# Optimization experiments

Measured on AMD Instinct MI355X. Metric: run time of the kernel, lower is better.

The kernel has to match this reference:

```python
import jax, jax.numpy as jnp
import numpy as np

B, H, S, D = 4, 16, 2048, 64
ROPE_BASE = 10000.0


def _rope(x):
    # Rotate-half RoPE over the last dim, positions along the second-to-last dim.
    d = x.shape[-1]
    s = x.shape[-2]
    inv_freq = 1.0 / (ROPE_BASE ** (jnp.arange(0, d, 2, dtype=jnp.float32) / d))  # [D/2]
    ang = jnp.arange(s, dtype=jnp.float32)[:, None] * inv_freq                    # [S, D/2]
    cos, sin = jnp.cos(ang), jnp.sin(ang)
    x1, x2 = x[..., : d // 2], x[..., d // 2:]
    return jnp.concatenate([x1 * cos - x2 * sin, x1 * sin + x2 * cos], axis=-1).astype(x.dtype)


def setup_inputs() -> dict:
    key = jax.random.key(0)
    kq, kk, kv = jax.random.split(key, 3)
    q = jax.random.normal(kq, (B, H, S, D), dtype=jnp.float32)
    k = jax.random.normal(kk, (B, H, S, D), dtype=jnp.float32)
    v = jax.random.normal(kv, (B, H, S, D), dtype=jnp.float32)
    mask = jnp.tril(jnp.ones((S, S), dtype=bool))  # causal, broadcasts over [B,H,S,S]
    return {"q": q, "k": k, "v": v, "mask": mask}


def reference(q, k, v, mask):
    d_k = q.shape[-1]
    qr = _rope(q)
    kr = _rope(k)
    scores = jnp.einsum('bhqd,bhkd->bhqk', qr, kr) / jnp.sqrt(jnp.asarray(d_k, jnp.float32))
    scores = jnp.where(mask, scores, -jnp.inf)  # masked_fill(mask == False, -inf)
    probs = jax.nn.softmax(scores, axis=-1)
    return jnp.einsum('bhqk,bhkd->bhqd', probs, v)
```

## Files before the change

kernel.cpp:

```cpp
#include <hip/hip_runtime.h>
#include <hip/hip_bf16.h>
#include <math.h>

#define SS 2048
#define DD 64
#define BH 64
#define KT 64
#define NT 256
#define NKT (SS / KT)
#define QTT 128
#define NTA 512
#define NQT (SS / QTT)
#define LQ 72
#define LOG2E 1.4426950408889634f
#define IFS (13.287712379549449f / 32.0f)

typedef __attribute__((ext_vector_type(8))) short s8v;
typedef __attribute__((ext_vector_type(4))) short s4v;
typedef __attribute__((ext_vector_type(4))) float f4v;

__device__ __forceinline__ short f2b(float x) {
  __hip_bfloat16 h = __float2bfloat16(x);
  return *reinterpret_cast<short*>(&h);
}

__device__ __forceinline__ void gload16(const void* g, void* l) {
  __builtin_amdgcn_global_load_lds(
      (const __attribute__((address_space(1))) void*)g,
      (__attribute__((address_space(3))) void*)l, 16, 0, 0);
}

template <int CTRL>
__device__ __forceinline__ float dppf(float x) {
  int i = __builtin_bit_cast(int, x);
  i = __builtin_amdgcn_update_dpp(i, i, CTRL, 0xf, 0xf, false);
  return __builtin_bit_cast(float, i);
}
__device__ __forceinline__ float rowmax16(float x) {
  x = fmaxf(x, dppf<0xB1>(x));
  x = fmaxf(x, dppf<0x4E>(x));
  x = fmaxf(x, dppf<0x124>(x));
  x = fmaxf(x, dppf<0x128>(x));
  return x;
}
__device__ __forceinline__ float rowsum16(float x) {
  x += dppf<0xB1>(x);
  x += dppf<0x4E>(x);
  x += dppf<0x124>(x);
  x += dppf<0x128>(x);
  return x;
}

__device__ __forceinline__ void rope_cs(int pos, int j, float& c, float& s) {
  float inv = exp2f(-(float)j * IFS);
  float ang = (float)pos * inv;
  __sincosf(ang, &s, &c);
}

__global__ __launch_bounds__(NT) void prep_kv_kernel(
    const float* __restrict__ kg, const float* __restrict__ vg,
    short* __restrict__ kr, short* __restrict__ vt) {
  __shared__ float Vs[KT][DD + 1];
  const int b = blockIdx.x;
  const int kt = b & 31;
  const int t = threadIdx.x;
  const size_t ofs = (size_t)b * (KT * DD);
  const float* ktile = kg + ofs;
  short* krt = kr + ofs;

#pragma unroll
  for (int i = 0; i < 8; ++i) {
    int idx = t + i * NT;
    int r = idx >> 5, j = idx & 31;
    float s, c;
    rope_cs(kt * KT + r, j, c, s);
    float x1 = ktile[r * DD + j], x2 = ktile[r * DD + j + 32];
    krt[r * DD + j] = f2b(x1 * c - x2 * s);
    krt[r * DD + j + 32] = f2b(x1 * s + x2 * c);
  }

  const float* vtile = vg + ofs;
#pragma unroll
  for (int i = 0; i < 4; ++i) {
    int s4 = t + i * NT;
    int r = s4 >> 4, c4 = (s4 & 15) * 4;
    float4 v = *(const float4*)&vtile[r * DD + c4];
    Vs[r][c4 + 0] = v.x;
    Vs[r][c4 + 1] = v.y;
    Vs[r][c4 + 2] = v.z;
    Vs[r][c4 + 3] = v.w;
  }
  __syncthreads();
  short* otile = vt + ofs;
#pragma unroll
  for (int i = 0; i < 2; ++i) {
    int c = t + i * NT;
    int d = c >> 3, k8 = (c & 7) * 8;
    s8v o;
#pragma unroll
    for (int u = 0; u < 8; ++u) {
      int kp = k8 + u;
      int src = ((kp & 3) << 4) + (kp >> 2);
      o[u] = f2b(Vs[src][d]);
    }
    *(s8v*)&otile[d * KT + k8] = o;
  }
}

__global__ __launch_bounds__(NTA, 6) void attn_fast(
    const float* __restrict__ qg, const short* __restrict__ kr,
    const short* __restrict__ vt, float* __restrict__ og) {
  __shared__ __align__(16) short Ks[2][KT * DD];
  __shared__ __align__(16) short Vts[2][DD * KT];
  __shared__ __align__(16) short QP[QTT * DD];

  const int tid = threadIdx.x;
  const int lane = tid & 63;
  const int wv = tid >> 6;
  const int quad = lane >> 4;
  const int lx = lane & 15;
  const int xb = lx & 7;
  const int foff0 = ((quad ^ xb) << 3);
  const int foff1 = (((quad | 4) ^ xb) << 3);

  const int bid = blockIdx.x;
  const int qb = (NQT - 1) - (bid >> 6);
  const int bh = bid & 63;
  const int qbase = qb * QTT;
  const int ktmax = 2 * qb + 1;
  const float* Q = qg + (size_t)bh * SS * DD;
  float* O = og + (size_t)bh * SS * DD;
  const short* krh = kr + (size_t)bh * SS * DD;
  const short* vth = vt + (size_t)bh * SS * DD;

  const int r_dma = tid >> 3;
  const int qs_dma = (tid & 7) ^ (r_dma & 7);
  const int goff = r_dma * DD + qs_dma * 8;
  const int loff = wv * 512;

  gload16(krh + goff, &Ks[0][loff]);
  gload16(vth + goff, &Vts[0][loff]);

  const float qscale = 0.125f * LOG2E;
#pragma unroll
  for (int t = 0; t < 8; ++t) {
    int idx = tid + t * NTA;
    int r = idx >> 5, j = idx & 31;
    float s, c;
    rope_cs(qbase + r, j, c, s);
    float x1 = Q[(size_t)(qbase + r) * DD + j];
    float x2 = Q[(size_t)(qbase + r) * DD + j + 32];
    int rb = r & 7;
    QP[r * DD + ((((j >> 3) ^ rb) << 3) | (j & 7))] = f2b((x1 * c - x2 * s) * qscale);
    QP[r * DD + (((((j >> 3) | 4) ^ rb) << 3) | (j & 7))] = f2b((x1 * s + x2 * c) * qscale);
  }
  __syncthreads();

  const int rq = wv * 16 + lx;
  s8v qf0 = *(const s8v*)&QP[rq * DD + foff0];
  s8v qf1 = *(const s8v*)&QP[rq * DD + foff1];

  const short bone = f2b(1.0f);
  s8v ones;
#pragma unroll
  for (int u = 0; u < 8; ++u) ones[u] = bone;

  short* Ps = &QP[wv * 16 * DD];

  f4v o_[4];
  f4v ol = (f4v){0.f, 0.f, 0.f, 0.f};
#pragma unroll
  for (int db = 0; db < 4; ++db) o_[db] = (f4v){0.f, 0.f, 0.f, 0.f};

  for (int kt = 0; kt <= ktmax; ++kt) {
    const int cur = kt & 1;
    if (kt) __syncthreads();

    if (kt < ktmax) {
      const short* ktile = krh + (size_t)(kt + 1) * (KT * DD);
      const short* vtile = vth + (size_t)(kt + 1) * (DD * KT);
      const int nxt = cur ^ 1;
      gload16(ktile + goff, &Ks[nxt][loff]);
      gload16(vtile + goff, &Vts[nxt][loff]);
    }

    f4v sc[4];
#pragma unroll
    for (int nb = 0; nb < 4; ++nb) {
      const int rk = nb * 16 + lx;
      s8v kf0 = *(const s8v*)&Ks[cur][rk * DD + foff0];
      s8v kf1 = *(const s8v*)&Ks[cur][rk * DD + foff1];
      f4v z = (f4v){0.f, 0.f, 0.f, 0.f};
      z = __builtin_amdgcn_mfma_f32_16x16x32_bf16(qf0, kf0, z, 0, 0, 0);
      z = __builtin_amdgcn_mfma_f32_16x16x32_bf16(qf1, kf1, z, 0, 0, 0);
      sc[nb] = z;
    }

    if (kt >= ktmax - 1) {
      const int kb = kt * KT;
#pragma unroll
      for (int nb = 0; nb < 4; ++nb)
#pragma unroll
        for (int r = 0; r < 4; ++r)
          if (kb + nb * 16 + lx > qbase + wv * 16 + quad * 4 + r) sc[nb][r] = -INFINITY;
    }

#pragma unroll
    for (int r = 0; r < 4; ++r) {
      const int rl = quad * 4 + r;
      float p0 = __builtin_amdgcn_exp2f(sc[0][r]);
      float p1 = __builtin_amdgcn_exp2f(sc[1][r]);
      float p2 = __builtin_amdgcn_exp2f(sc[2][r]);
      float p3 = __builtin_amdgcn_exp2f(sc[3][r]);
      s4v pk = {f2b(p0), f2b(p1), f2b(p2), f2b(p3)};
      *(s4v*)&Ps[rl * DD + (((lx >> 1) ^ (rl & 7)) << 3) + ((lx & 1) << 2)] = pk;
    }

    s8v pf0 = *(const s8v*)&Ps[lx * DD + foff0];
    s8v pf1 = *(const s8v*)&Ps[lx * DD + foff1];
    ol = __builtin_amdgcn_mfma_f32_16x16x32_bf16(pf0, ones, ol, 0, 0, 0);
    ol = __builtin_amdgcn_mfma_f32_16x16x32_bf16(pf1, ones, ol, 0, 0, 0);
#pragma unroll
    for (int db = 0; db < 4; ++db) {
      const int rv = db * 16 + lx;
      s8v vf0 = *(const s8v*)&Vts[cur][rv * KT + foff0];
      s8v vf1 = *(const s8v*)&Vts[cur][rv * KT + foff1];
      o_[db] = __builtin_amdgcn_mfma_f32_16x16x32_bf16(pf0, vf0, o_[db], 0, 0, 0);
      o_[db] = __builtin_amdgcn_mfma_f32_16x16x32_bf16(pf1, vf1, o_[db], 0, 0, 0);
    }
  }

#pragma unroll
  for (int r = 0; r < 4; ++r) {
    float rinv = 1.0f / ol[r];
    int row = qbase + wv * 16 + quad * 4 + r;
#pragma unroll
    for (int db = 0; db < 4; ++db)
      O[(size_t)row * DD + db * 16 + lx] = o_[db][r] * rinv;
  }
}

__global__ __launch_bounds__(NT, 4) void attn_fallback(
    const float* __restrict__ qg, const float* __restrict__ kg,
    const float* __restrict__ vg, float* __restrict__ og) {
  __shared__ __align__(16) short Qs[64 * LQ];
  __shared__ __align__(16) short Ksh[64 * LQ];
  __shared__ __align__(16) short Vt[DD * LQ];
  __shared__ __align__(16) short Ps[4][16 * LQ];

  const int tid = threadIdx.x;
  const int lane = tid & 63;
  const int wv = tid >> 6;
  const int quad = lane >> 4;
  const int lx = lane & 15;

  const int bid = blockIdx.x;
  const int qt = NKT - 1 - (bid >> 6);
  const int bh = bid & 63;
  const int qbase = qt * 64;
  const size_t base = (size_t)bh * SS * DD;
  const float* Q = qg + base;
  const float* K = kg + base;
  const float* V = vg + base;
  float* O = og + base;

  const float qscale = 0.125f * LOG2E;
  for (int t = 0; t < 8; ++t) {
    int idx = tid + t * NT;
    int r = idx >> 5, j = idx & 31;
    float c, s;
    rope_cs(qbase + r, j, c, s);
    float x1 = Q[(size_t)(qbase + r) * DD + j];
    float x2 = Q[(size_t)(qbase + r) * DD + j + 32];
    Qs[r * LQ + j] = f2b((x1 * c - x2 * s) * qscale);
    Qs[r * LQ + j + 32] = f2b((x1 * s + x2 * c) * qscale);
  }
  __syncthreads();

  s8v qf0 = *(const s8v*)&Qs[(wv * 16 + lx) * LQ + quad * 8];
  s8v qf1 = *(const s8v*)&Qs[(wv * 16 + lx) * LQ + 32 + quad * 8];

  float m_[4], l_[4];
  f4v o_[4];
#pragma unroll
  for (int r = 0; r < 4; ++r) { m_[r] = -INFINITY; l_[r] = 0.f; }
#pragma unroll
  for (int db = 0; db < 4; ++db) o_[db] = (f4v){0.f, 0.f, 0.f, 0.f};

  for (int kt = 0; kt <= qt; ++kt) {
    const int kbase = kt * 64;
    __syncthreads();
    for (int t = 0; t < 8; ++t) {
      int idx = tid + t * NT;
      int r = idx >> 5, j = idx & 31;
      float c, s;
      rope_cs(kbase + r, j, c, s);
      float x1 = K[(size_t)(kbase + r) * DD + j];
      float x2 = K[(size_t)(kbase + r) * DD + j + 32];
      Ksh[r * LQ + j] = f2b(x1 * c - x2 * s);
      Ksh[r * LQ + j + 32] = f2b(x1 * s + x2 * c);
    }
    for (int t = 0; t < 4; ++t) {
      int i4 = tid + t * NT;
      int r = i4 >> 4, c4 = (i4 & 15) * 4;
      const float4 v = *(const float4*)&V[(size_t)(kbase + r) * DD + c4];
      Vt[(c4 + 0) * LQ + r] = f2b(v.x);
      Vt[(c4 + 1) * LQ + r] = f2b(v.y);
      Vt[(c4 + 2) * LQ + r] = f2b(v.z);
      Vt[(c4 + 3) * LQ + r] = f2b(v.w);
    }
    __syncthreads();

    f4v sc[4];
#pragma unroll
    for (int nb = 0; nb < 4; ++nb) {
      s8v kf0 = *(const s8v*)&Ksh[(nb * 16 + lx) * LQ + quad * 8];
      s8v kf1 = *(const s8v*)&Ksh[(nb * 16 + lx) * LQ + 32 + quad * 8];
      f4v z = (f4v){0.f, 0.f, 0.f, 0.f};
      z = __builtin_amdgcn_mfma_f32_16x16x32_bf16(qf0, kf0, z, 0, 0, 0);
      z = __builtin_amdgcn_mfma_f32_16x16x32_bf16(qf1, kf1, z, 0, 0, 0);
      sc[nb] = z;
    }
    if (kt == qt) {
#pragma unroll
      for (int nb = 0; nb < 4; ++nb)
#pragma unroll
        for (int r = 0; r < 4; ++r)
          if (kbase + nb * 16 + lx > qbase + wv * 16 + quad * 4 + r)
            sc[nb][r] = -INFINITY;
    }
#pragma unroll
    for (int r = 0; r < 4; ++r) {
      float mx = fmaxf(fmaxf(sc[0][r], sc[1][r]), fmaxf(sc[2][r], sc[3][r]));
      mx = rowmax16(mx);
      float mn = fmaxf(m_[r], mx);
      float al = __builtin_amdgcn_exp2f(m_[r] - mn);
      m_[r] = mn;
      float rs = 0.f;
#pragma unroll
      for (int nb = 0; nb < 4; ++nb) {
        float p = __builtin_amdgcn_exp2f(sc[nb][r] - mn);
        rs += p;
        Ps[wv][(quad * 4 + r) * LQ + nb * 16 + lx] = f2b(p);
      }
      rs = rowsum16(rs);
      l_[r] = l_[r] * al + rs;
      o_[0][r] *= al; o_[1][r] *= al; o_[2][r] *= al; o_[3][r] *= al;
    }
    s8v pf0 = *(const s8v*)&Ps[wv][lx * LQ + quad * 8];
    s8v pf1 = *(const s8v*)&Ps[wv][lx * LQ + 32 + quad * 8];
#pragma unroll
    for (int db = 0; db < 4; ++db) {
      s8v vf0 = *(const s8v*)&Vt[(db * 16 + lx) * LQ + quad * 8];
      s8v vf1 = *(const s8v*)&Vt[(db * 16 + lx) * LQ + 32 + quad * 8];
      o_[db] = __builtin_amdgcn_mfma_f32_16x16x32_bf16(pf0, vf0, o_[db], 0, 0, 0);
      o_[db] = __builtin_amdgcn_mfma_f32_16x16x32_bf16(pf1, vf1, o_[db], 0, 0, 0);
    }
  }
#pragma unroll
  for (int r = 0; r < 4; ++r) {
    float rinv = 1.0f / l_[r];
    int row = qbase + wv * 16 + quad * 4 + r;
#pragma unroll
    for (int db = 0; db < 4; ++db)
      O[(size_t)row * DD + db * 16 + lx] = o_[db][r] * rinv;
  }
}

extern "C" void kernel_launch(void* const* d_in, const int* in_sizes, int n_in,
                              void* d_out, int out_size, void* d_ws, size_t ws_size,
                              hipStream_t stream) {
  const float* q = (const float*)d_in[0];
  const float* k = (const float*)d_in[1];
  const float* v = (const float*)d_in[2];
  float* out = (float*)d_out;

  const size_t kr_bytes = (size_t)BH * SS * DD * sizeof(short);
  const size_t vt_bytes = kr_bytes;
  const size_t need = kr_bytes + vt_bytes;

  if (ws_size >= need) {
    short* kr = (short*)d_ws;
    short* vt = (short*)((char*)d_ws + kr_bytes);
    prep_kv_kernel<<<BH * NKT, NT, 0, stream>>>(k, v, kr, vt);
    attn_fast<<<dim3(BH * NQT), dim3(NTA), 0, stream>>>(q, kr, vt, out);
  } else {
    attn_fallback<<<dim3(BH * NKT), dim3(NT), 0, stream>>>(q, k, v, out);
  }
}
```

Measured before the change: 192.4 us.

## Double query tile to 256 rows per block with per-wave causal skipping

The query tile per block grows from 128 to 256 rows, with each wave handling two 16-row halves so every K/V tile loaded into LDS feeds twice as many MFMAs. Each wave now skips K tiles beyond its own causal diagonal, and block ordering interleaves heavy and light query blocks for load balance. The QP buffer doubles, and launch bounds drop to 4 blocks per SM because of the higher register and LDS use. The cost is fewer resident blocks, a smaller grid, and waves in a block that sit idle during the last tiles.

```diff
diff --git a/kernel.cpp b/kernel.cpp
--- a/kernel.cpp
+++ b/kernel.cpp
@@ -8,7 +8,7 @@
 #define KT 64
 #define NT 256
 #define NKT (SS / KT)
-#define QTT 128
+#define QTT 256
 #define NTA 512
 #define NQT (SS / QTT)
 #define LQ 72
@@ -107,7 +107,7 @@
   }
 }
 
-__global__ __launch_bounds__(NTA, 6) void attn_fast(
+__global__ __launch_bounds__(NTA, 4) void attn_fast(
     const float* __restrict__ qg, const short* __restrict__ kr,
     const short* __restrict__ vt, float* __restrict__ og) {
   __shared__ __align__(16) short Ks[2][KT * DD];
@@ -124,10 +124,12 @@
   const int foff1 = (((quad | 4) ^ xb) << 3);
 
   const int bid = blockIdx.x;
-  const int qb = (NQT - 1) - (bid >> 6);
+  const int g = bid >> 6;
+  const int qb = (g < 4) ? (7 - g) : (g - 4);
   const int bh = bid & 63;
   const int qbase = qb * QTT;
-  const int ktmax = 2 * qb + 1;
+  const int ktmax = 4 * qb + 3;
+  const int mykt = 4 * qb + (wv >> 1);
   const float* Q = qg + (size_t)bh * SS * DD;
   float* O = og + (size_t)bh * SS * DD;
   const short* krh = kr + (size_t)bh * SS * DD;
@@ -143,7 +145,7 @@
 
   const float qscale = 0.125f * LOG2E;
 #pragma unroll
-  for (int t = 0; t < 8; ++t) {
+  for (int t = 0; t < 16; ++t) {
     int idx = tid + t * NTA;
     int r = idx >> 5, j = idx & 31;
     float s, c;
@@ -156,21 +158,29 @@
   }
   __syncthreads();
 
-  const int rq = wv * 16 + lx;
-  s8v qf0 = *(const s8v*)&QP[rq * DD + foff0];
-  s8v qf1 = *(const s8v*)&QP[rq * DD + foff1];
+  s8v qf0[2], qf1[2];
+#pragma unroll
+  for (int h = 0; h < 2; ++h) {
+    const int rq = wv * 32 + h * 16 + lx;
+    qf0[h] = *(const s8v*)&QP[rq * DD + foff0];
+    qf1[h] = *(const s8v*)&QP[rq * DD + foff1];
+  }
 
   const short bone = f2b(1.0f);
   s8v ones;
 #pragma unroll
   for (int u = 0; u < 8; ++u) ones[u] = bone;
 
-  short* Ps = &QP[wv * 16 * DD];
-
-  f4v o_[4];
-  f4v ol = (f4v){0.f, 0.f, 0.f, 0.f};
-#pragma unroll
-  for (int db = 0; db < 4; ++db) o_[db] = (f4v){0.f, 0.f, 0.f, 0.f};
+  short* Ps = &QP[wv * 32 * DD];
+
+  f4v o_[2][4];
+  f4v ol[2];
+#pragma unroll
+  for (int h = 0; h < 2; ++h) {
+    ol[h] = (f4v){0.f, 0.f, 0.f, 0.f};
+#pragma unroll
+    for (int db = 0; db < 4; ++db) o_[h][db] = (f4v){0.f, 0.f, 0.f, 0.f};
+  }
 
   for (int kt = 0; kt <= ktmax; ++kt) {
     const int cur = kt & 1;
@@ -184,60 +194,81 @@
       gload16(vtile + goff, &Vts[nxt][loff]);
     }
 
-    f4v sc[4];
-#pragma unroll
-    for (int nb = 0; nb < 4; ++nb) {
-      const int rk = nb * 16 + lx;
-      s8v kf0 = *(const s8v*)&Ks[cur][rk * DD + foff0];
-      s8v kf1 = *(const s8v*)&Ks[cur][rk * DD + foff1];
-      f4v z = (f4v){0.f, 0.f, 0.f, 0.f};
-      z = __builtin_amdgcn_mfma_f32_16x16x32_bf16(qf0, kf0, z, 0, 0, 0);
-      z = __builtin_amdgcn_mfma_f32_16x16x32_bf16(qf1, kf1, z, 0, 0, 0);
-      sc[nb] = z;
-    }
-
-    if (kt >= ktmax - 1) {
-      const int kb = kt * KT;
-#pragma unroll
-      for (int nb = 0; nb < 4; ++nb)
-#pragma unroll
-        for (int r = 0; r < 4; ++r)
-          if (kb + nb * 16 + lx > qbase + wv * 16 + quad * 4 + r) sc[nb][r] = -INFINITY;
-    }
-
+    if (kt <= mykt) {
+      f4v sc[2][4];
+#pragma unroll
+      for (int nb = 0; nb < 4; ++nb) {
+        const int rk = nb * 16 + lx;
+        s8v kf0 = *(const s8v*)&Ks[cur][rk * DD + foff0];
+        s8v kf1 = *(const s8v*)&Ks[cur][rk * DD + foff1];
+#pragma unroll
+        for (int h = 0; h < 2; ++h) {
+          f4v z = (f4v){0.f, 0.f, 0.f, 0.f};
+          z = __builtin_amdgcn_mfma_f32_16x16x32_bf16(qf0[h], kf0, z, 0, 0, 0);
+          z = __builtin_amdgcn_mfma_f32_16x16x32_bf16(qf1[h], kf1, z, 0, 0, 0);
+          sc[h][nb] = z;
+        }
+      }
+
+      if (kt == mykt) {
+        const int kb = kt * KT;
+#pragma unroll
+        for (int h = 0; h < 2; ++h) {
+          const int qrow = qbase + wv * 32 + h * 16 + quad * 4;
+#pragma unroll
+          for (int nb = 0; nb < 4; ++nb)
+#pragma unroll
+            for (int r = 0; r < 4; ++r)
+              if (kb + nb * 16 + lx > qrow + r) sc[h][nb][r] = -INFINITY;
+        }
+      }
+
+#pragma unroll
+      for (int h = 0; h < 2; ++h) {
+#pragma unroll
+        for (int r = 0; r < 4; ++r) {
+          const int rl = quad * 4 + r;
+          float p0 = __builtin_amdgcn_exp2f(sc[h][0][r]);
+          float p1 = __builtin_amdgcn_exp2f(sc[h][1][r]);
+          float p2 = __builtin_amdgcn_exp2f(sc[h][2][r]);
+          float p3 = __builtin_amdgcn_exp2f(sc[h][3][r]);
+          s4v pk = {f2b(p0), f2b(p1), f2b(p2), f2b(p3)};
+          *(s4v*)&Ps[(h * 16 + rl) * DD + (((lx >> 1) ^ (rl & 7)) << 3) + ((lx & 1) << 2)] = pk;
+        }
+      }
+
+      s8v pf0[2], pf1[2];
+#pragma unroll
+      for (int h = 0; h < 2; ++h) {
+        pf0[h] = *(const s8v*)&Ps[(h * 16 + lx) * DD + foff0];
+        pf1[h] = *(const s8v*)&Ps[(h * 16 + lx) * DD + foff1];
+        ol[h] = __builtin_amdgcn_mfma_f32_16x16x32_bf16(pf0[h], ones, ol[h], 0, 0, 0);
+        ol[h] = __builtin_amdgcn_mfma_f32_16x16x32_bf16(pf1[h], ones, ol[h], 0, 0, 0);
+      }
+#pragma unroll
+      for (int db = 0; db < 4; ++db) {
+        const int rv = db * 16 + lx;
+        s8v vf0 = *(const s8v*)&Vts[cur][rv * KT + foff0];
+        s8v vf1 = *(const s8v*)&Vts[cur][rv * KT + foff1];
+#pragma unroll
+        for (int h = 0; h < 2; ++h) {
+          o_[h][db] = __builtin_amdgcn_mfma_f32_16x16x32_bf16(pf0[h], vf0, o_[h][db], 0, 0, 0);
+          o_[h][db] = __builtin_amdgcn_mfma_f32_16x16x32_bf16(pf1[h], vf1, o_[h][db], 0, 0, 0);
+        }
+      }
+    }
+  }
+
+#pragma unroll
+  for (int h = 0; h < 2; ++h)
 #pragma unroll
     for (int r = 0; r < 4; ++r) {
-      const int rl = quad * 4 + r;
-      float p0 = __builtin_amdgcn_exp2f(sc[0][r]);
-      float p1 = __builtin_amdgcn_exp2f(sc[1][r]);
-      float p2 = __builtin_amdgcn_exp2f(sc[2][r]);
-      float p3 = __builtin_amdgcn_exp2f(sc[3][r]);
-      s4v pk = {f2b(p0), f2b(p1), f2b(p2), f2b(p3)};
-      *(s4v*)&Ps[rl * DD + (((lx >> 1) ^ (rl & 7)) << 3) + ((lx & 1) << 2)] = pk;
-    }
-
-    s8v pf0 = *(const s8v*)&Ps[lx * DD + foff0];
-    s8v pf1 = *(const s8v*)&Ps[lx * DD + foff1];
-    ol = __builtin_amdgcn_mfma_f32_16x16x32_bf16(pf0, ones, ol, 0, 0, 0);
-    ol = __builtin_amdgcn_mfma_f32_16x16x32_bf16(pf1, ones, ol, 0, 0, 0);
-#pragma unroll
-    for (int db = 0; db < 4; ++db) {
-      const int rv = db * 16 + lx;
-      s8v vf0 = *(const s8v*)&Vts[cur][rv * KT + foff0];
-      s8v vf1 = *(const s8v*)&Vts[cur][rv * KT + foff1];
-      o_[db] = __builtin_amdgcn_mfma_f32_16x16x32_bf16(pf0, vf0, o_[db], 0, 0, 0);
-      o_[db] = __builtin_amdgcn_mfma_f32_16x16x32_bf16(pf1, vf1, o_[db], 0, 0, 0);
-    }
-  }
-
-#pragma unroll
-  for (int r = 0; r < 4; ++r) {
-    float rinv = 1.0f / ol[r];
-    int row = qbase + wv * 16 + quad * 4 + r;
-#pragma unroll
-    for (int db = 0; db < 4; ++db)
-      O[(size_t)row * DD + db * 16 + lx] = o_[db][r] * rinv;
-  }
+      float rinv = 1.0f / ol[h][r];
+      int row = qbase + wv * 32 + h * 16 + quad * 4 + r;
+#pragma unroll
+      for (int db = 0; db < 4; ++db)
+        O[(size_t)row * DD + db * 16 + lx] = o_[h][db][r] * rinv;
+    }
 }
 
 __global__ __launch_bounds__(NT, 4) void attn_fallback(
```

Measured after the change: 186.1 us. 1.03x faster.
